# Optimization experiments

Hardware: AMD Instinct MI355X
Metric: run time of the kernel (lower is better)

The kernel has to match this reference:

```python
import jax, jax.numpy as jnp
import numpy as np

N_NODES = 100000
N_EDGES = 6400000
N_GRAPHS = 512
IN_DIM, HID, OUT = 4, 64, 128


def setup_inputs() -> dict:
    key = jax.random.key(0)
    ks = jax.random.split(key, 6)
    x = jax.random.normal(ks[0], (N_NODES, IN_DIM), dtype=jnp.float32)
    edge_index = jax.random.randint(ks[1], (2, N_EDGES), 0, N_NODES, dtype=jnp.int64)
    batch_ids = jnp.sort(jax.random.randint(ks[2], (N_NODES,), 0, N_GRAPHS, dtype=jnp.int64))
    W1 = jax.random.normal(ks[3], (IN_DIM, HID), dtype=jnp.float32) * (1.0 / np.sqrt(IN_DIM))
    b1 = jnp.zeros((HID,), dtype=jnp.float32)
    W2 = jax.random.normal(ks[4], (HID, HID), dtype=jnp.float32) * (1.0 / np.sqrt(HID))
    b2 = jnp.zeros((HID,), dtype=jnp.float32)
    Wlin = jax.random.normal(ks[5], (HID, OUT), dtype=jnp.float32) * (1.0 / np.sqrt(HID))
    blin = jnp.zeros((OUT,), dtype=jnp.float32)
    return {"x": x, "edge_index": edge_index, "batch_ids": batch_ids,
            "W1": W1, "b1": b1, "W2": W2, "b2": b2, "Wlin": Wlin, "blin": blin}


def reference(x, edge_index, batch_ids, W1, b1, W2, b2, Wlin, blin):
    # GINConv (eps=0): agg[v] = sum_{(u->v) in E} x[u];  h = MLP(x + agg)
    src, dst = edge_index[0], edge_index[1]
    agg = jax.ops.segment_sum(x[src], dst, num_segments=N_NODES)  # [N, in_dim]
    h = x + agg
    h = jax.nn.relu(h @ W1 + b1)  # [N, hid]
    h = h @ W2 + b2               # [N, hid]
    # global mean pool over graphs
    sums = jax.ops.segment_sum(h, batch_ids, num_segments=N_GRAPHS)  # [G, hid]
    counts = jax.ops.segment_sum(jnp.ones((h.shape[0],), dtype=h.dtype), batch_ids,
                                 num_segments=N_GRAPHS)
    pooled = sums / jnp.maximum(counts, 1.0)[:, None]  # [G, hid]
    return pooled @ Wlin + blin  # [G, out]
```

## Files before the change

### kernel.cpp

```cpp
#include <hip/hip_runtime.h>
#include <hip/hip_bf16.h>

#define N_NODES  100000
#define N_EDGES  6400000
#define N_GRAPHS 512
#define HID      64
#define OUT_DIM  128

#define BIN_SHIFT 6
#define BIN_NODES 64
#define NB 1563
#define CAP 5120
#define MAXSEG 8

#define SCB 512
#define SCT 1024
#define SCH (N_EDGES / SCB)
#define SEGB ((NB + 15) / 16)
#define ITERS 13

#define BMT 512
#define NW  8

__global__ void __launch_bounds__(SCT)
scatter_bin(const int* __restrict__ src, const int* __restrict__ dst,
            unsigned int* __restrict__ cursor, unsigned int* __restrict__ binned) {
    __shared__ unsigned int hist[NB];
    __shared__ unsigned int gbase[NB];
    __shared__ unsigned int sorted[SCH];
    __shared__ unsigned int wtot[16];

    const int tid = threadIdx.x, lane = tid & 63, w = tid >> 6;
    const int e0 = blockIdx.x * SCH;

    int dreg[ITERS], sreg[ITERS];
    #pragma unroll
    for (int k = 0; k < ITERS; ++k) {
        int idx = k * SCT + tid;
        if (idx < SCH) { dreg[k] = dst[e0 + idx]; sreg[k] = src[e0 + idx]; }
        else           { dreg[k] = -1;            sreg[k] = 0; }
    }

    for (int i = tid; i < NB; i += SCT) hist[i] = 0u;
    __syncthreads();

    #pragma unroll
    for (int k = 0; k < ITERS; ++k)
        if (dreg[k] >= 0) atomicAdd(&hist[dreg[k] >> BIN_SHIFT], 1u);
    __syncthreads();

    const int s0 = w * SEGB;
    const int s1 = min(s0 + SEGB, NB);
    unsigned int carry = 0u;
    for (int base = s0; base < s1; base += 64) {
        int i = base + lane;
        bool ok = (i < s1);
        unsigned int v = ok ? hist[i] : 0u;
        if (ok && v)
            gbase[i] = (unsigned int)i * CAP + atomicAdd(&cursor[i], v);
        unsigned int xi = v;
        #pragma unroll
        for (int d = 1; d < 64; d <<= 1) {
            unsigned int u = __shfl_up(xi, d, 64);
            if (lane >= d) xi += u;
        }
        if (ok) hist[i] = carry + xi - v;
        carry += __shfl(xi, 63, 64);
    }
    if (lane == 0) wtot[w] = carry;
    __syncthreads();
    if (w == 0 && lane < 16) {
        unsigned int v = wtot[lane], xi = v;
        #pragma unroll
        for (int d = 1; d < 16; d <<= 1) {
            unsigned int u = __shfl_up(xi, d, 64);
            if (lane >= d) xi += u;
        }
        wtot[lane] = xi - v;
    }
    __syncthreads();
    {
        unsigned int woff = wtot[w];
        for (int i = s0 + lane; i < s1; i += 64) hist[i] += woff;
    }
    __syncthreads();

    #pragma unroll
    for (int k = 0; k < ITERS; ++k) {
        if (dreg[k] >= 0) {
            int b = dreg[k] >> BIN_SHIFT;
            unsigned int slot = atomicAdd(&hist[b], 1u);
            sorted[slot] = ((unsigned int)sreg[k] << BIN_SHIFT)
                         | (unsigned int)(dreg[k] & (BIN_NODES - 1));
        }
    }
    __syncthreads();

    const int sub = lane >> 3, le = lane & 7;
    for (int bb = s0 + sub; bb < s1; bb += 8) {
        unsigned int lo = (bb == 0) ? 0u : hist[bb - 1];
        unsigned int hi = hist[bb];
        unsigned int len = hi - lo;
        if (len == 0u) continue;
        unsigned int gb  = gbase[bb];
        unsigned int end = (unsigned int)(bb + 1) * CAP;
        for (unsigned int t = le; t < len; t += 8)
            if (gb + t < end) binned[gb + t] = sorted[lo + t];
    }
}

__global__ void __launch_bounds__(BMT)
bin_mlp_pool(const unsigned int* __restrict__ binned,
             const unsigned int* __restrict__ cursor,
             const float* __restrict__ x, const int* __restrict__ batch,
             const float* __restrict__ W1, const float* __restrict__ b1,
             float* __restrict__ gsum, float* __restrict__ gcnt) {
    const int b   = blockIdx.x;
    const int n0  = b << BIN_SHIFT;
    const int tid = threadIdx.x;
    const int lane = tid & 63;
    const int w    = tid >> 6;

    __shared__ unsigned int hist[BIN_NODES];
    __shared__ unsigned int off[BIN_NODES + 1];
    __shared__ unsigned int run[BIN_NODES];
    __shared__ unsigned int ssrc[CAP];
    __shared__ float lagg[BIN_NODES][4];
    __shared__ float psum[NW][MAXSEG][HID];
    __shared__ float pcnt[NW][MAXSEG];

    if (tid < BIN_NODES) hist[tid] = 0u;
    for (int i = tid; i < NW * MAXSEG * HID; i += BMT) ((float*)psum)[i] = 0.0f;
    if (tid < NW * MAXSEG) ((float*)pcnt)[tid] = 0.0f;
    __syncthreads();

    unsigned int cnt = cursor[b];
    if (cnt > CAP) cnt = CAP;
    const unsigned int* bp = binned + (size_t)b * CAP;

    for (unsigned int i = tid; i < cnt; i += BMT)
        atomicAdd(&hist[bp[i] & (BIN_NODES - 1)], 1u);
    __syncthreads();

    if (tid < BIN_NODES) {
        unsigned int v = hist[tid];
        #pragma unroll
        for (int d = 1; d < 64; d <<= 1) {
            unsigned int u = __shfl_up(v, d, 64);
            if (lane >= d) v += u;
        }
        off[tid + 1] = v;
        if (tid == 0) off[0] = 0u;
        run[tid] = 0u;
    }
    __syncthreads();

    for (unsigned int i = tid; i < cnt; i += BMT) {
        unsigned int p = bp[i];
        unsigned int dl = p & (BIN_NODES - 1);
        unsigned int slot = off[dl] + atomicAdd(&run[dl], 1u);
        ssrc[slot] = p >> BIN_SHIFT;
    }
    __syncthreads();

    {
        const int sub = lane >> 4, sl = lane & 15;
        #pragma unroll
        for (int r = 0; r < 2; ++r) {
            int dl = w * 8 + r * 4 + sub;
            unsigned int o0 = off[dl], o1 = off[dl + 1];
            float a0 = 0.f, a1 = 0.f, a2 = 0.f, a3 = 0.f;
            for (unsigned int i = o0 + sl; i < o1; i += 16) {
                unsigned int s = ssrc[i];
                float4 xv = *reinterpret_cast<const float4*>(x + (size_t)s * 4);
                a0 += xv.x; a1 += xv.y; a2 += xv.z; a3 += xv.w;
            }
            #pragma unroll
            for (int d = 8; d >= 1; d >>= 1) {
                a0 += __shfl_xor(a0, d, 16);
                a1 += __shfl_xor(a1, d, 16);
                a2 += __shfl_xor(a2, d, 16);
                a3 += __shfl_xor(a3, d, 16);
            }
            if (sl == 0) {
                lagg[dl][0] = a0; lagg[dl][1] = a1;
                lagg[dl][2] = a2; lagg[dl][3] = a3;
            }
        }
    }
    __syncthreads();

    const int j = lane;
    const float w1c0 = W1[0 * HID + j], w1c1 = W1[1 * HID + j];
    const float w1c2 = W1[2 * HID + j], w1c3 = W1[3 * HID + j];
    const float b1j = b1[j];
    const int base_g = batch[n0];

    for (int vl = w * 8; vl < w * 8 + 8; ++vl) {
        int v = n0 + vl;
        if (v >= N_NODES) break;
        float xa0 = x[(size_t)v * 4 + 0] + lagg[vl][0];
        float xa1 = x[(size_t)v * 4 + 1] + lagg[vl][1];
        float xa2 = x[(size_t)v * 4 + 2] + lagg[vl][2];
        float xa3 = x[(size_t)v * 4 + 3] + lagg[vl][3];
        float h = b1j;
        h = fmaf(xa0, w1c0, h);
        h = fmaf(xa1, w1c1, h);
        h = fmaf(xa2, w1c2, h);
        h = fmaf(xa3, w1c3, h);
        h = fmaxf(h, 0.0f);
        int g = batch[v];
        int seg = g - base_g;
        if (seg < MAXSEG) {
            psum[w][seg][j] += h;
            if (j == 0) pcnt[w][seg] += 1.0f;
        } else {
            unsafeAtomicAdd(&gsum[(size_t)g * HID + j], h);
            if (j == 0) unsafeAtomicAdd(&gcnt[g], 1.0f);
        }
    }
    __syncthreads();

    {
        int seg = w;
        float v8 = 0.0f;
        #pragma unroll
        for (int r = 0; r < NW; ++r) v8 += psum[r][seg][j];
        if (v8 != 0.0f)
            unsafeAtomicAdd(&gsum[(size_t)(base_g + seg) * HID + j], v8);
    }
    if (tid < MAXSEG) {
        float c = 0.0f;
        #pragma unroll
        for (int r = 0; r < NW; ++r) c += pcnt[r][tid];
        if (c > 0.0f)
            unsafeAtomicAdd(&gcnt[base_g + tid], c);
    }
}

__global__ void finalize(const float* __restrict__ gsum, const float* __restrict__ gcnt,
                         const float* __restrict__ W2, const float* __restrict__ b2,
                         const float* __restrict__ Wlin, const float* __restrict__ blin,
                         float* __restrict__ out) {
    int g = blockIdx.x;
    int j = threadIdx.x;
    __shared__ float pooled[HID];

    float cnt = gcnt[g];
    float inv = 1.0f / fmaxf(cnt, 1.0f);

    if (j < HID) {
        float s = cnt * b2[j];
        #pragma unroll 8
        for (int k = 0; k < HID; ++k)
            s = fmaf(gsum[(size_t)g * HID + k], W2[k * HID + j], s);
        pooled[j] = s * inv;
    }
    __syncthreads();

    float o = blin[j];
    #pragma unroll 8
    for (int k = 0; k < HID; ++k)
        o = fmaf(pooled[k], Wlin[k * OUT_DIM + j], o);
    out[(size_t)g * OUT_DIM + j] = o;
}

__global__ void edge_scatter(const int* __restrict__ src, const int* __restrict__ dst,
                             const float* __restrict__ x, float* __restrict__ agg) {
    int stride = gridDim.x * blockDim.x;
    for (int e = blockIdx.x * blockDim.x + threadIdx.x; e < N_EDGES; e += stride) {
        int s = src[e];
        int d = dst[e];
        float4 xv = *reinterpret_cast<const float4*>(x + (size_t)s * 4);
        float* a = agg + (size_t)d * 4;
        unsafeAtomicAdd(a + 0, xv.x);
        unsafeAtomicAdd(a + 1, xv.y);
        unsafeAtomicAdd(a + 2, xv.z);
        unsafeAtomicAdd(a + 3, xv.w);
    }
}

__global__ void node_mlp_pool(const float* __restrict__ x, const float* __restrict__ agg,
                              const int* __restrict__ batch,
                              const float* __restrict__ W1, const float* __restrict__ b1,
                              float* __restrict__ gsum, float* __restrict__ gcnt) {
    int j = threadIdx.x & 63;
    int local = threadIdx.x >> 6;
    int v = blockIdx.x * 4 + local;
    if (v >= N_NODES) return;
    float4 xv = *reinterpret_cast<const float4*>(x + (size_t)v * 4);
    float4 av = *reinterpret_cast<const float4*>(agg + (size_t)v * 4);
    float h = b1[j];
    h = fmaf(xv.x + av.x, W1[0 * HID + j], h);
    h = fmaf(xv.y + av.y, W1[1 * HID + j], h);
    h = fmaf(xv.z + av.z, W1[2 * HID + j], h);
    h = fmaf(xv.w + av.w, W1[3 * HID + j], h);
    h = fmaxf(h, 0.0f);
    int g = batch[v];
    unsafeAtomicAdd(&gsum[(size_t)g * HID + j], h);
    if (j == 0) unsafeAtomicAdd(&gcnt[g], 1.0f);
}

extern "C" void kernel_launch(void* const* d_in, const int* in_sizes, int n_in,
                              void* d_out, int out_size, void* d_ws, size_t ws_size,
                              hipStream_t stream) {
    const float* x    = (const float*)d_in[0];
    const int*   ei   = (const int*)d_in[1];
    const int*   bat  = (const int*)d_in[2];
    const float* W1   = (const float*)d_in[3];
    const float* b1   = (const float*)d_in[4];
    const float* W2   = (const float*)d_in[5];
    const float* b2   = (const float*)d_in[6];
    const float* Wlin = (const float*)d_in[7];
    const float* blin = (const float*)d_in[8];
    float* out = (float*)d_out;

    const int* src  = ei;
    const int* dstp = ei + N_EDGES;

    char* ws = (char*)d_ws;
    const size_t GSUM_OFF = 0, GCNT_OFF = 131072, CUR_OFF = 133120, BIN_OFF = 139392;
    const size_t NEED = BIN_OFF + (size_t)NB * CAP * 4;

    if (ws_size >= NEED) {
        float* gsum = (float*)(ws + GSUM_OFF);
        float* gcnt = (float*)(ws + GCNT_OFF);
        unsigned int* cursor = (unsigned int*)(ws + CUR_OFF);
        unsigned int* binned = (unsigned int*)(ws + BIN_OFF);

        hipMemsetAsync(d_ws, 0, BIN_OFF, stream);

        scatter_bin<<<SCB, SCT, 0, stream>>>(src, dstp, cursor, binned);
        bin_mlp_pool<<<NB, BMT, 0, stream>>>(binned, cursor, x, bat, W1, b1, gsum, gcnt);
        finalize<<<N_GRAPHS, OUT_DIM, 0, stream>>>(gsum, gcnt, W2, b2, Wlin, blin, out);
    } else {
        float* agg  = (float*)(ws);
        float* gsum = (float*)(ws + 1600000);
        float* gcnt = (float*)(ws + 1600000 + 131072);
        hipMemsetAsync(d_ws, 0, 1600000 + 131072 + 2048, stream);
        edge_scatter<<<4096, 256, 0, stream>>>(src, dstp, x, agg);
        node_mlp_pool<<<(N_NODES + 3) / 4, 256, 0, stream>>>(x, agg, bat, W1, b1, gsum, gcnt);
        finalize<<<N_GRAPHS, OUT_DIM, 0, stream>>>(gsum, gcnt, W2, b2, Wlin, blin, out);
    }
}
```

Baseline: 90.57 us.

## Pack atomic ranks into registers to halve shared-memory atomics in binning

Both binning stages now keep the rank returned by the first histogram atomicAdd, packed into the upper bits of the edge word held in registers. The second pass computes its slot as prefix offset plus rank, so the second round of LDS atomics and the reload of binned data from global memory go away. The bin kernel also loads edges as uint4 into registers, capped at C4*4*BMT = 6144 entries, which covers CAP = 5120. This depends on source ids fitting in 17 bits and ranks fitting in the remaining upper bits, and it adds register pressure.

```diff
diff --git a/kernel.cpp b/kernel.cpp
--- a/kernel.cpp
+++ b/kernel.cpp
@@ -21,6 +21,7 @@
 
 #define BMT 512
 #define NW  8
+#define C4 3
 
 __global__ void __launch_bounds__(SCT)
 scatter_bin(const int* __restrict__ src, const int* __restrict__ dst,
@@ -33,12 +34,12 @@
     const int tid = threadIdx.x, lane = tid & 63, w = tid >> 6;
     const int e0 = blockIdx.x * SCH;
 
-    int dreg[ITERS], sreg[ITERS];
+    int dreg[ITERS]; unsigned int sreg[ITERS];
     #pragma unroll
     for (int k = 0; k < ITERS; ++k) {
         int idx = k * SCT + tid;
-        if (idx < SCH) { dreg[k] = dst[e0 + idx]; sreg[k] = src[e0 + idx]; }
-        else           { dreg[k] = -1;            sreg[k] = 0; }
+        if (idx < SCH) { dreg[k] = dst[e0 + idx]; sreg[k] = (unsigned int)src[e0 + idx]; }
+        else           { dreg[k] = -1;            sreg[k] = 0u; }
     }
 
     for (int i = tid; i < NB; i += SCT) hist[i] = 0u;
@@ -46,7 +47,10 @@
 
     #pragma unroll
     for (int k = 0; k < ITERS; ++k)
-        if (dreg[k] >= 0) atomicAdd(&hist[dreg[k] >> BIN_SHIFT], 1u);
+        if (dreg[k] >= 0) {
+            unsigned int r = atomicAdd(&hist[dreg[k] >> BIN_SHIFT], 1u);
+            sreg[k] |= (r << 20);
+        }
     __syncthreads();
 
     const int s0 = w * SEGB;
@@ -89,17 +93,18 @@
     for (int k = 0; k < ITERS; ++k) {
         if (dreg[k] >= 0) {
             int b = dreg[k] >> BIN_SHIFT;
-            unsigned int slot = atomicAdd(&hist[b], 1u);
-            sorted[slot] = ((unsigned int)sreg[k] << BIN_SHIFT)
-                         | (unsigned int)(dreg[k] & (BIN_NODES - 1));
+            unsigned int rank = sreg[k] >> 20;
+            unsigned int s17  = sreg[k] & 0x1FFFFu;
+            sorted[hist[b] + rank] = (s17 << BIN_SHIFT)
+                                   | (unsigned int)(dreg[k] & (BIN_NODES - 1));
         }
     }
     __syncthreads();
 
     const int sub = lane >> 3, le = lane & 7;
     for (int bb = s0 + sub; bb < s1; bb += 8) {
-        unsigned int lo = (bb == 0) ? 0u : hist[bb - 1];
-        unsigned int hi = hist[bb];
+        unsigned int lo = hist[bb];
+        unsigned int hi = (bb + 1 < NB) ? hist[bb + 1] : (unsigned int)SCH;
         unsigned int len = hi - lo;
         if (len == 0u) continue;
         unsigned int gb  = gbase[bb];
@@ -123,7 +128,6 @@
 
     __shared__ unsigned int hist[BIN_NODES];
     __shared__ unsigned int off[BIN_NODES + 1];
-    __shared__ unsigned int run[BIN_NODES];
     __shared__ unsigned int ssrc[CAP];
     __shared__ float lagg[BIN_NODES][4];
     __shared__ float psum[NW][MAXSEG][HID];
@@ -138,8 +142,25 @@
     if (cnt > CAP) cnt = CAP;
     const unsigned int* bp = binned + (size_t)b * CAP;
 
-    for (unsigned int i = tid; i < cnt; i += BMT)
-        atomicAdd(&hist[bp[i] & (BIN_NODES - 1)], 1u);
+    unsigned int breg[C4][4];
+    #pragma unroll
+    for (int k = 0; k < C4; ++k) {
+        unsigned int i0 = (unsigned int)k * (BMT * 4) + (unsigned int)(tid << 2);
+        if (i0 < cnt) {
+            uint4 v4 = *reinterpret_cast<const uint4*>(bp + i0);
+            breg[k][0] = v4.x; breg[k][1] = v4.y;
+            breg[k][2] = v4.z; breg[k][3] = v4.w;
+            #pragma unroll
+            for (int j = 0; j < 4; ++j) {
+                if (i0 + j < cnt) {
+                    unsigned int r = atomicAdd(&hist[breg[k][j] & (BIN_NODES - 1)], 1u);
+                    breg[k][j] |= (r << 23);
+                } else breg[k][j] = 0xFFFFFFFFu;
+            }
+        } else {
+            breg[k][0] = breg[k][1] = breg[k][2] = breg[k][3] = 0xFFFFFFFFu;
+        }
+    }
     __syncthreads();
 
     if (tid < BIN_NODES) {
@@ -151,16 +172,20 @@
         }
         off[tid + 1] = v;
         if (tid == 0) off[0] = 0u;
-        run[tid] = 0u;
-    }
-    __syncthreads();
-
-    for (unsigned int i = tid; i < cnt; i += BMT) {
-        unsigned int p = bp[i];
-        unsigned int dl = p & (BIN_NODES - 1);
-        unsigned int slot = off[dl] + atomicAdd(&run[dl], 1u);
-        ssrc[slot] = p >> BIN_SHIFT;
-    }
+    }
+    __syncthreads();
+
+    #pragma unroll
+    for (int k = 0; k < C4; ++k)
+        #pragma unroll
+        for (int j = 0; j < 4; ++j) {
+            unsigned int e = breg[k][j];
+            if (e != 0xFFFFFFFFu) {
+                unsigned int dl   = e & (BIN_NODES - 1);
+                unsigned int rank = e >> 23;
+                ssrc[off[dl] + rank] = (e >> BIN_SHIFT) & 0x1FFFFu;
+            }
+        }
     __syncthreads();
 
     {
@@ -320,7 +345,7 @@
 
     char* ws = (char*)d_ws;
     const size_t GSUM_OFF = 0, GCNT_OFF = 131072, CUR_OFF = 133120, BIN_OFF = 139392;
-    const size_t NEED = BIN_OFF + (size_t)NB * CAP * 4;
+    const size_t NEED = BIN_OFF + (size_t)NB * CAP * 4 + 16384;
 
     if (ws_size >= NEED) {
         float* gsum = (float*)(ws + GSUM_OFF);
```

After: 94.23 us. 1.04x slower.

## Replace global bin cursors with per-block sorted runs and run-info table

Applied to the files above, without the earlier changes.

The scatter kernel no longer reserves space in global per-bin buckets with atomics. Each block writes its locally sorted edges contiguously, plus a table of (offset,length) per bin per block. The consumer kernel has each of its 512 threads read one block's run for its bin. This removes global atomics and the scattered writes, but consumer reads become a serial per-thread loop over short strided runs, which may coalesce poorly.

```diff
diff --git a/kernel.cpp b/kernel.cpp
--- a/kernel.cpp
+++ b/kernel.cpp
@@ -24,9 +24,8 @@
 
 __global__ void __launch_bounds__(SCT)
 scatter_bin(const int* __restrict__ src, const int* __restrict__ dst,
-            unsigned int* __restrict__ cursor, unsigned int* __restrict__ binned) {
+            unsigned int* __restrict__ runinfo, unsigned int* __restrict__ binned) {
     __shared__ unsigned int hist[NB];
-    __shared__ unsigned int gbase[NB];
     __shared__ unsigned int sorted[SCH];
     __shared__ unsigned int wtot[16];
 
@@ -56,8 +55,6 @@
         int i = base + lane;
         bool ok = (i < s1);
         unsigned int v = ok ? hist[i] : 0u;
-        if (ok && v)
-            gbase[i] = (unsigned int)i * CAP + atomicAdd(&cursor[i], v);
         unsigned int xi = v;
         #pragma unroll
         for (int d = 1; d < 64; d <<= 1) {
@@ -96,22 +93,24 @@
     }
     __syncthreads();
 
-    const int sub = lane >> 3, le = lane & 7;
-    for (int bb = s0 + sub; bb < s1; bb += 8) {
-        unsigned int lo = (bb == 0) ? 0u : hist[bb - 1];
-        unsigned int hi = hist[bb];
-        unsigned int len = hi - lo;
-        if (len == 0u) continue;
-        unsigned int gb  = gbase[bb];
-        unsigned int end = (unsigned int)(bb + 1) * CAP;
-        for (unsigned int t = le; t < len; t += 8)
-            if (gb + t < end) binned[gb + t] = sorted[lo + t];
+    {
+        unsigned int* dstp = binned + (size_t)blockIdx.x * SCH;
+        #pragma unroll
+        for (int k = 0; k < ITERS; ++k) {
+            int i = k * SCT + tid;
+            if (i < SCH) dstp[i] = sorted[i];
+        }
+        for (int i = tid; i < NB; i += SCT) {
+            unsigned int lo = (i == 0) ? 0u : hist[i - 1];
+            unsigned int len = hist[i] - lo;
+            runinfo[(size_t)i * SCB + blockIdx.x] = (lo << 16) | len;
+        }
     }
 }
 
 __global__ void __launch_bounds__(BMT)
 bin_mlp_pool(const unsigned int* __restrict__ binned,
-             const unsigned int* __restrict__ cursor,
+             const unsigned int* __restrict__ runinfo,
              const float* __restrict__ x, const int* __restrict__ batch,
              const float* __restrict__ W1, const float* __restrict__ b1,
              float* __restrict__ gsum, float* __restrict__ gcnt) {
@@ -134,12 +133,12 @@
     if (tid < NW * MAXSEG) ((float*)pcnt)[tid] = 0.0f;
     __syncthreads();
 
-    unsigned int cnt = cursor[b];
-    if (cnt > CAP) cnt = CAP;
-    const unsigned int* bp = binned + (size_t)b * CAP;
-
-    for (unsigned int i = tid; i < cnt; i += BMT)
-        atomicAdd(&hist[bp[i] & (BIN_NODES - 1)], 1u);
+    unsigned int ri = runinfo[(size_t)b * SCB + tid];
+    const unsigned int* base = binned + (size_t)tid * SCH + (ri >> 16);
+    unsigned int len = ri & 0xFFFFu;
+
+    for (unsigned int i = 0; i < len; ++i)
+        atomicAdd(&hist[base[i] & (BIN_NODES - 1)], 1u);
     __syncthreads();
 
     if (tid < BIN_NODES) {
@@ -155,11 +154,11 @@
     }
     __syncthreads();
 
-    for (unsigned int i = tid; i < cnt; i += BMT) {
-        unsigned int p = bp[i];
+    for (unsigned int i = 0; i < len; ++i) {
+        unsigned int p = base[i];
         unsigned int dl = p & (BIN_NODES - 1);
         unsigned int slot = off[dl] + atomicAdd(&run[dl], 1u);
-        ssrc[slot] = p >> BIN_SHIFT;
+        if (slot < CAP) ssrc[slot] = p >> BIN_SHIFT;
     }
     __syncthreads();
 
@@ -168,7 +167,8 @@
         #pragma unroll
         for (int r = 0; r < 2; ++r) {
             int dl = w * 8 + r * 4 + sub;
-            unsigned int o0 = off[dl], o1 = off[dl + 1];
+            unsigned int o0 = min(off[dl],     (unsigned int)CAP);
+            unsigned int o1 = min(off[dl + 1], (unsigned int)CAP);
             float a0 = 0.f, a1 = 0.f, a2 = 0.f, a3 = 0.f;
             for (unsigned int i = o0 + sl; i < o1; i += 16) {
                 unsigned int s = ssrc[i];
@@ -319,19 +319,20 @@
     const int* dstp = ei + N_EDGES;
 
     char* ws = (char*)d_ws;
-    const size_t GSUM_OFF = 0, GCNT_OFF = 131072, CUR_OFF = 133120, BIN_OFF = 139392;
-    const size_t NEED = BIN_OFF + (size_t)NB * CAP * 4;
+    const size_t GSUM_OFF = 0, GCNT_OFF = 131072, RI_OFF = 133120;
+    const size_t BIN_OFF  = RI_OFF + (size_t)NB * SCB * 4;
+    const size_t NEED = BIN_OFF + (size_t)SCB * SCH * 4;
 
     if (ws_size >= NEED) {
         float* gsum = (float*)(ws + GSUM_OFF);
         float* gcnt = (float*)(ws + GCNT_OFF);
-        unsigned int* cursor = (unsigned int*)(ws + CUR_OFF);
-        unsigned int* binned = (unsigned int*)(ws + BIN_OFF);
-
-        hipMemsetAsync(d_ws, 0, BIN_OFF, stream);
-
-        scatter_bin<<<SCB, SCT, 0, stream>>>(src, dstp, cursor, binned);
-        bin_mlp_pool<<<NB, BMT, 0, stream>>>(binned, cursor, x, bat, W1, b1, gsum, gcnt);
+        unsigned int* runinfo = (unsigned int*)(ws + RI_OFF);
+        unsigned int* binned  = (unsigned int*)(ws + BIN_OFF);
+
+        hipMemsetAsync(d_ws, 0, RI_OFF, stream);
+
+        scatter_bin<<<SCB, SCT, 0, stream>>>(src, dstp, runinfo, binned);
+        bin_mlp_pool<<<NB, BMT, 0, stream>>>(binned, runinfo, x, bat, W1, b1, gsum, gcnt);
         finalize<<<N_GRAPHS, OUT_DIM, 0, stream>>>(gsum, gcnt, W2, b2, Wlin, blin, out);
     } else {
         float* agg  = (float*)(ws);
```

Measured after the change: 157.7 us. +74.1%, slower.
